# Kernel optimization log

Hardware: AMD Instinct MI355X
Metric: run time of the kernel (lower is better)

The kernel has to match this reference:

```python
import jax, jax.numpy as jnp
import numpy as np

N = 250000
E = 4000000
IN_F, HID, OUT = 18, 16, 1


def setup_inputs() -> dict:
    key = jax.random.key(0)
    ks = jax.random.split(key, 7)
    x = jax.random.normal(ks[0], (N, IN_F), dtype=jnp.float32)
    edge_index = jax.random.randint(ks[1], (2, E), 0, N, dtype=jnp.int64)
    # GCNConv params (PyG uses Glorot for weight, zeros for bias)
    W1 = jax.random.normal(ks[2], (IN_F, HID), dtype=jnp.float32) * (1.0 / np.sqrt(IN_F))
    b1 = jnp.zeros((HID,), dtype=jnp.float32)
    W2 = jax.random.normal(ks[3], (HID, OUT), dtype=jnp.float32) * (1.0 / np.sqrt(HID))
    b2 = jnp.zeros((OUT,), dtype=jnp.float32)
    return {"x": x, "edge_index": edge_index, "W1": W1, "b1": b1, "W2": W2, "b2": b2}


def _gcn_conv(x, W, b, src, dst, norm, n_nodes):
    # linear transform then degree-normalized scatter-add (PyG GCNConv)
    h = x @ W                                  # [N, F_out]
    msg = h[src] * norm[:, None]               # gather + per-edge scale
    out = jax.ops.segment_sum(msg, dst, num_segments=n_nodes)
    return out + b


def reference(x, edge_index, W1, b1, W2, b2):
    # add self-loops (GCNConv default add_self_loops=True)
    loops = jnp.arange(N, dtype=edge_index.dtype)
    src = jnp.concatenate([edge_index[0], loops])
    dst = jnp.concatenate([edge_index[1], loops])
    # symmetric normalization: deg computed at destination over self-looped graph
    deg = jax.ops.segment_sum(jnp.ones_like(dst, dtype=x.dtype), dst, num_segments=N)
    dis = jnp.where(deg > 0, jax.lax.rsqrt(deg), 0.0)
    norm = dis[src] * dis[dst]                 # [E+N]
    h = _gcn_conv(x, W1, b1, src, dst, norm, N)
    h = jax.nn.relu(h)
    # dropout is identity in eval mode (F.dropout(training=self.training))
    out = _gcn_conv(h, W2, b2, src, dst, norm, N)
    return out
```

## Files before the change

### kernel.cpp

```cpp
#include <hip/hip_runtime.h>
#include <hip/hip_fp16.h>


#define NB_BITS 8
#define BN (1 << NB_BITS)
#define NBINS 1024
#define BIN_TPB 512
#define BIN_CHUNK 8192
#define AGG_TPB 512
#define UF 8

__global__ void bhist_kernel(const int* __restrict__ dst, int* __restrict__ bcnt, int E) {
    __shared__ int cnt[NBINS];
    int t = threadIdx.x;
    for (int i = t; i < NBINS; i += BIN_TPB) cnt[i] = 0;
    __syncthreads();
    int base = blockIdx.x * BIN_CHUNK;
    int end = min(base + BIN_CHUNK, E);
#pragma unroll 4
    for (int e = base + t; e < end; e += BIN_TPB)
        atomicAdd(&cnt[dst[e] >> NB_BITS], 1);
    __syncthreads();
    for (int i = t; i < NBINS; i += BIN_TPB)
        if (cnt[i] > 0) atomicAdd(&bcnt[i], cnt[i]);
}

__global__ void bscan_kernel(const int* __restrict__ bcnt, int* __restrict__ bstart,
                             int* __restrict__ cursor) {
    __shared__ int s[NBINS];
    int t = threadIdx.x;
    int v = bcnt[t];
    s[t] = v;
    __syncthreads();
    for (int off = 1; off < NBINS; off <<= 1) {
        int add = (t >= off) ? s[t - off] : 0;
        __syncthreads();
        s[t] += add;
        __syncthreads();
    }
    int excl = s[t] - v;
    bstart[t] = excl;
    cursor[t] = excl;
    if (t == NBINS - 1) bstart[NBINS] = s[t];
}

__global__ void bplace_kernel(const int* __restrict__ src, const int* __restrict__ dst,
                              int* __restrict__ cursor, int* __restrict__ pairs, int E) {
    __shared__ int cnt[NBINS];
    int t = threadIdx.x;
    for (int i = t; i < NBINS; i += BIN_TPB) cnt[i] = 0;
    __syncthreads();
    int base = blockIdx.x * BIN_CHUNK;
    int end = min(base + BIN_CHUNK, E);
#pragma unroll 4
    for (int e = base + t; e < end; e += BIN_TPB)
        atomicAdd(&cnt[dst[e] >> NB_BITS], 1);
    __syncthreads();
    for (int i = t; i < NBINS; i += BIN_TPB) {
        int c = cnt[i];
        cnt[i] = (c > 0) ? atomicAdd(&cursor[i], c) : 0;
    }
    __syncthreads();
#pragma unroll 4
    for (int e = base + t; e < end; e += BIN_TPB) {
        int d = dst[e];
        int sv = src[e];
        int b = d >> NB_BITS;
        int p = atomicAdd(&cnt[b], 1);
        pairs[p] = (sv << NB_BITS) | (d & (BN - 1));
    }
}

__global__ void csr_kernel(const int* __restrict__ pairs, const int* __restrict__ bstart,
                           int* __restrict__ rowp, int* __restrict__ csr_src,
                           float* __restrict__ dis, int N) {
    __shared__ int cnt[BN];
    __shared__ int tmp[BN];
    int b = blockIdx.x, t = threadIdx.x;
    int s0 = bstart[b], s1 = bstart[b + 1];
    for (int i = t; i < BN; i += blockDim.x) cnt[i] = 0;
    __syncthreads();
#pragma unroll 4
    for (int e = s0 + t; e < s1; e += blockDim.x)
        atomicAdd(&cnt[pairs[e] & (BN - 1)], 1);
    __syncthreads();
    int v = (t < BN) ? cnt[t] : 0;
    if (t < BN) tmp[t] = v;
    __syncthreads();
    for (int off = 1; off < BN; off <<= 1) {
        int add = (t < BN && t >= off) ? tmp[t - off] : 0;
        __syncthreads();
        if (t < BN) tmp[t] += add;
        __syncthreads();
    }
    int nbase = b << NB_BITS;
    if (t < BN) {
        int start = s0 + tmp[t] - v;
        rowp[nbase + t] = start;
        int n = nbase + t;
        if (n < N) dis[n] = rsqrtf((float)v + 1.0f);
        cnt[t] = start;
    }
    if (t == 0) rowp[nbase + BN] = s1;
    __syncthreads();
#pragma unroll 4
    for (int e = s0 + t; e < s1; e += blockDim.x) {
        int pv = pairs[e];
        int pos = atomicAdd(&cnt[pv & (BN - 1)], 1);
        csr_src[pos] = pv >> NB_BITS;
    }
}

__global__ void h1_kernel(const float* __restrict__ x, const float* __restrict__ W1,
                          const float* __restrict__ dis, __half* __restrict__ hs1h, int N) {
    __shared__ float w[18 * 16];
    for (int i = threadIdx.x; i < 18 * 16; i += blockDim.x) w[i] = W1[i];
    __syncthreads();
    int n = blockIdx.x * blockDim.x + threadIdx.x;
    if (n >= N) return;
    const float2* x2 = (const float2*)(x + (size_t)n * 18);
    float xv[18];
#pragma unroll
    for (int k = 0; k < 9; k++) {
        float2 v = x2[k];
        xv[2 * k] = v.x;
        xv[2 * k + 1] = v.y;
    }
    float d = dis[n];
    float acc[16];
#pragma unroll
    for (int f = 0; f < 16; f++) acc[f] = 0.0f;
#pragma unroll
    for (int k = 0; k < 18; k++) {
        float xk = xv[k];
#pragma unroll
        for (int f = 0; f < 16; f++) acc[f] = fmaf(xk, w[k * 16 + f], acc[f]);
    }
    unsigned int u[8];
#pragma unroll
    for (int q = 0; q < 8; q++) {
        unsigned int lo = __half_as_ushort(__float2half_rn(acc[2 * q] * d));
        unsigned int hi = __half_as_ushort(__float2half_rn(acc[2 * q + 1] * d));
        u[q] = lo | (hi << 16);
    }
    uint4* outp = (uint4*)(hs1h + (size_t)n * 16);
    outp[0] = make_uint4(u[0], u[1], u[2], u[3]);
    outp[1] = make_uint4(u[4], u[5], u[6], u[7]);
}

__global__ void agg1_kernel(const int* __restrict__ csr_src, const int* __restrict__ rowp,
                            const __half* __restrict__ hs1h, const float* __restrict__ dis,
                            const float* __restrict__ b1, const float* __restrict__ W2,
                            float* __restrict__ hs2, int N) {
    int b = blockIdx.x, t = threadIdx.x;
    int f = t & 15;
    int g = t >> 4;
    float bbf = b1[f], wwf = W2[f];
    int nbase = b << NB_BITS;
    for (int nl = g; nl < BN; nl += AGG_TPB / 16) {
        int n = nbase + nl;
        if (n >= N) continue;
        int r0 = rowp[n], r1 = rowp[n + 1];
        float a = 0.f;
#pragma unroll 4
        for (int r = r0; r < r1; ++r) {
            int s = csr_src[r];
            a += __half2float(hs1h[(size_t)s * 16 + f]);
        }
        float d = dis[n];
        float self = __half2float(hs1h[(size_t)n * 16 + f]);
        float p = fmaxf(d * (a + self) + bbf, 0.f) * wwf;
        p += __shfl_xor(p, 1);
        p += __shfl_xor(p, 2);
        p += __shfl_xor(p, 4);
        p += __shfl_xor(p, 8);
        if (f == 0) hs2[n] = p * d;
    }
}

__global__ void agg2_kernel(const int* __restrict__ csr_src, const int* __restrict__ rowp,
                            const float* __restrict__ hs2, const float* __restrict__ dis,
                            const float* __restrict__ b2, float* __restrict__ out, int N) {
    int b = blockIdx.x, t = threadIdx.x;
    int l = t & 15;
    int g = t >> 4;
    int nbase = b << NB_BITS;
    float bb = b2[0];
    for (int nl = g; nl < BN; nl += AGG_TPB / 16) {
        int n = nbase + nl;
        if (n >= N) continue;
        int r0 = rowp[n], r1 = rowp[n + 1];
        float a = 0.f;
        for (int r = r0 + l; r < r1; r += 16) a += hs2[csr_src[r]];
        a += __shfl_xor(a, 1);
        a += __shfl_xor(a, 2);
        a += __shfl_xor(a, 4);
        a += __shfl_xor(a, 8);
        if (l == 0) out[n] = dis[n] * (a + hs2[n]) + bb;
    }
}

extern "C" void kernel_launch(void* const* d_in, const int* in_sizes, int n_in,
                              void* d_out, int out_size, void* d_ws, size_t ws_size,
                              hipStream_t stream) {
    const float* x = (const float*)d_in[0];
    const int* edge_index = (const int*)d_in[1];
    const float* W1 = (const float*)d_in[2];
    const float* b1 = (const float*)d_in[3];
    const float* W2 = (const float*)d_in[4];
    const float* b2 = (const float*)d_in[5];
    float* out = (float*)d_out;

    const int N = in_sizes[0] / 18;
    const int E = in_sizes[1] / 2;
    const int* src = edge_index;
    const int* dst = edge_index + E;
    const int NBUCKET = (N + BN - 1) / BN;

    int* ws = (int*)d_ws;
    int* pairs = ws;
    int* csr_src = pairs + (size_t)E;
    __half* hs1h = (__half*)(csr_src + (size_t)E);
    float* hs2 = (float*)((int*)(csr_src + (size_t)E) + 8 * (size_t)N);
    float* dis = hs2 + N;
    int* rowp = (int*)(dis + N);
    int* bstart = rowp + (size_t)NBUCKET * BN + 1;
    int* cursor = bstart + NBINS + 1;
    int* bcnt = cursor + NBINS;

    hipMemsetAsync(bcnt, 0, NBINS * sizeof(int), stream);

    int binBlocks = (E + BIN_CHUNK - 1) / BIN_CHUNK;
    int nBlocksN = (N + 255) / 256;

    bhist_kernel<<<binBlocks, BIN_TPB, 0, stream>>>(dst, bcnt, E);
    bscan_kernel<<<1, NBINS, 0, stream>>>(bcnt, bstart, cursor);
    bplace_kernel<<<binBlocks, BIN_TPB, 0, stream>>>(src, dst, cursor, pairs, E);
    csr_kernel<<<NBUCKET, 512, 0, stream>>>(pairs, bstart, rowp, csr_src, dis, N);
    h1_kernel<<<nBlocksN, 256, 0, stream>>>(x, W1, dis, hs1h, N);
    agg1_kernel<<<NBUCKET, AGG_TPB, 0, stream>>>(csr_src, rowp, hs1h, dis, b1, W2, hs2, N);
    agg2_kernel<<<NBUCKET, AGG_TPB, 0, stream>>>(csr_src, rowp, hs2, dis, b2, out, N);
}
```

Baseline: 276.8 us.

## Stage bucket placement in LDS and coarsen CSR buckets to 512 nodes

The binning pass now uses 512 coarse buckets of 512 nodes each, so each CSR block handles 512 nodes with one thread per node. In the placement kernel each block first sorts its chunk into LDS by bucket, using a local scan and per-bucket cursors. It then writes each bucket's entries as contiguous runs to global memory instead of scattering one word per edge. The aim is more coalesced writes and fewer global cursor atomics, at the cost of roughly 48KB of LDS per block (lower occupancy), an extra in-block scan, and more sync. The aggregation kernels keep 256-node blocks, which still works because rowp is indexed by node.

Result: faster. 254.1 us (-8.2%).

```diff
diff --git a/kernel.cpp b/kernel.cpp
--- a/kernel.cpp
+++ b/kernel.cpp
@@ -4,35 +4,35 @@
 
 #define NB_BITS 8
 #define BN (1 << NB_BITS)
-#define NBINS 1024
+#define SB_BITS 9
+#define SBN (1 << SB_BITS)
+#define NSB 512
 #define BIN_TPB 512
 #define BIN_CHUNK 8192
 #define AGG_TPB 512
-#define UF 8
 
 __global__ void bhist_kernel(const int* __restrict__ dst, int* __restrict__ bcnt, int E) {
-    __shared__ int cnt[NBINS];
+    __shared__ int cnt[NSB];
     int t = threadIdx.x;
-    for (int i = t; i < NBINS; i += BIN_TPB) cnt[i] = 0;
+    cnt[t] = 0;
     __syncthreads();
     int base = blockIdx.x * BIN_CHUNK;
     int end = min(base + BIN_CHUNK, E);
 #pragma unroll 4
     for (int e = base + t; e < end; e += BIN_TPB)
-        atomicAdd(&cnt[dst[e] >> NB_BITS], 1);
-    __syncthreads();
-    for (int i = t; i < NBINS; i += BIN_TPB)
-        if (cnt[i] > 0) atomicAdd(&bcnt[i], cnt[i]);
+        atomicAdd(&cnt[dst[e] >> SB_BITS], 1);
+    __syncthreads();
+    if (cnt[t] > 0) atomicAdd(&bcnt[t], cnt[t]);
 }
 
 __global__ void bscan_kernel(const int* __restrict__ bcnt, int* __restrict__ bstart,
                              int* __restrict__ cursor) {
-    __shared__ int s[NBINS];
+    __shared__ int s[NSB];
     int t = threadIdx.x;
     int v = bcnt[t];
     s[t] = v;
     __syncthreads();
-    for (int off = 1; off < NBINS; off <<= 1) {
+    for (int off = 1; off < NSB; off <<= 1) {
         int add = (t >= off) ? s[t - off] : 0;
         __syncthreads();
         s[t] += add;
@@ -41,73 +41,92 @@
     int excl = s[t] - v;
     bstart[t] = excl;
     cursor[t] = excl;
-    if (t == NBINS - 1) bstart[NBINS] = s[t];
+    if (t == NSB - 1) bstart[NSB] = s[t];
 }
 
 __global__ void bplace_kernel(const int* __restrict__ src, const int* __restrict__ dst,
                               int* __restrict__ cursor, int* __restrict__ pairs, int E) {
-    __shared__ int cnt[NBINS];
+    __shared__ int cnt[NSB];
+    __shared__ int lstart[NSB];
+    __shared__ int lcur[NSB];
+    __shared__ int gbase[NSB];
+    __shared__ int lbuf[BIN_CHUNK];
+    __shared__ unsigned short lbin[BIN_CHUNK];
     int t = threadIdx.x;
-    for (int i = t; i < NBINS; i += BIN_TPB) cnt[i] = 0;
-    __syncthreads();
     int base = blockIdx.x * BIN_CHUNK;
     int end = min(base + BIN_CHUNK, E);
+    cnt[t] = 0;
+    __syncthreads();
 #pragma unroll 4
     for (int e = base + t; e < end; e += BIN_TPB)
-        atomicAdd(&cnt[dst[e] >> NB_BITS], 1);
-    __syncthreads();
-    for (int i = t; i < NBINS; i += BIN_TPB) {
-        int c = cnt[i];
-        cnt[i] = (c > 0) ? atomicAdd(&cursor[i], c) : 0;
-    }
-    __syncthreads();
-#pragma unroll 4
+        atomicAdd(&cnt[dst[e] >> SB_BITS], 1);
+    __syncthreads();
+    int v = cnt[t];
+    lstart[t] = v;
+    __syncthreads();
+    for (int off = 1; off < NSB; off <<= 1) {
+        int add = (t >= off) ? lstart[t - off] : 0;
+        __syncthreads();
+        lstart[t] += add;
+        __syncthreads();
+    }
+    int excl = lstart[t] - v;
+    lstart[t] = excl;
+    lcur[t] = excl;
+    gbase[t] = (v > 0) ? atomicAdd(&cursor[t], v) : 0;
+    __syncthreads();
+#pragma unroll 2
     for (int e = base + t; e < end; e += BIN_TPB) {
-        int d = dst[e];
-        int sv = src[e];
-        int b = d >> NB_BITS;
-        int p = atomicAdd(&cnt[b], 1);
-        pairs[p] = (sv << NB_BITS) | (d & (BN - 1));
+        int d = dst[e], s = src[e];
+        int b = d >> SB_BITS;
+        int pos = atomicAdd(&lcur[b], 1);
+        lbuf[pos] = (s << SB_BITS) | (d & (SBN - 1));
+        lbin[pos] = (unsigned short)b;
+    }
+    __syncthreads();
+    int n = end - base;
+#pragma unroll 4
+    for (int i = t; i < n; i += BIN_TPB) {
+        int b = lbin[i];
+        pairs[gbase[b] + (i - lstart[b])] = lbuf[i];
     }
 }
 
 __global__ void csr_kernel(const int* __restrict__ pairs, const int* __restrict__ bstart,
                            int* __restrict__ rowp, int* __restrict__ csr_src,
                            float* __restrict__ dis, int N) {
-    __shared__ int cnt[BN];
-    __shared__ int tmp[BN];
+    __shared__ int cnt[SBN];
+    __shared__ int tmp[SBN];
     int b = blockIdx.x, t = threadIdx.x;
     int s0 = bstart[b], s1 = bstart[b + 1];
-    for (int i = t; i < BN; i += blockDim.x) cnt[i] = 0;
-    __syncthreads();
-#pragma unroll 4
-    for (int e = s0 + t; e < s1; e += blockDim.x)
-        atomicAdd(&cnt[pairs[e] & (BN - 1)], 1);
-    __syncthreads();
-    int v = (t < BN) ? cnt[t] : 0;
-    if (t < BN) tmp[t] = v;
-    __syncthreads();
-    for (int off = 1; off < BN; off <<= 1) {
-        int add = (t < BN && t >= off) ? tmp[t - off] : 0;
-        __syncthreads();
-        if (t < BN) tmp[t] += add;
-        __syncthreads();
-    }
-    int nbase = b << NB_BITS;
-    if (t < BN) {
-        int start = s0 + tmp[t] - v;
-        rowp[nbase + t] = start;
-        int n = nbase + t;
-        if (n < N) dis[n] = rsqrtf((float)v + 1.0f);
-        cnt[t] = start;
-    }
-    if (t == 0) rowp[nbase + BN] = s1;
-    __syncthreads();
-#pragma unroll 4
-    for (int e = s0 + t; e < s1; e += blockDim.x) {
+    cnt[t] = 0;
+    __syncthreads();
+#pragma unroll 4
+    for (int e = s0 + t; e < s1; e += SBN)
+        atomicAdd(&cnt[pairs[e] & (SBN - 1)], 1);
+    __syncthreads();
+    int v = cnt[t];
+    tmp[t] = v;
+    __syncthreads();
+    for (int off = 1; off < SBN; off <<= 1) {
+        int add = (t >= off) ? tmp[t - off] : 0;
+        __syncthreads();
+        tmp[t] += add;
+        __syncthreads();
+    }
+    int nbase = b << SB_BITS;
+    int start = s0 + tmp[t] - v;
+    rowp[nbase + t] = start;
+    int n = nbase + t;
+    if (n < N) dis[n] = rsqrtf((float)v + 1.0f);
+    cnt[t] = start;
+    if (t == 0) rowp[nbase + SBN] = s1;
+    __syncthreads();
+#pragma unroll 4
+    for (int e = s0 + t; e < s1; e += SBN) {
         int pv = pairs[e];
-        int pos = atomicAdd(&cnt[pv & (BN - 1)], 1);
-        csr_src[pos] = pv >> NB_BITS;
+        int pos = atomicAdd(&cnt[pv & (SBN - 1)], 1);
+        csr_src[pos] = pv >> SB_BITS;
     }
 }
 
@@ -215,7 +234,8 @@
     const int E = in_sizes[1] / 2;
     const int* src = edge_index;
     const int* dst = edge_index + E;
-    const int NBUCKET = (N + BN - 1) / BN;
+    const int NABUCKET = (N + BN - 1) / BN;
+    const int NSBUCKET = (N + SBN - 1) / SBN;
 
     int* ws = (int*)d_ws;
     int* pairs = ws;
@@ -224,20 +244,20 @@
     float* hs2 = (float*)((int*)(csr_src + (size_t)E) + 8 * (size_t)N);
     float* dis = hs2 + N;
     int* rowp = (int*)(dis + N);
-    int* bstart = rowp + (size_t)NBUCKET * BN + 1;
-    int* cursor = bstart + NBINS + 1;
-    int* bcnt = cursor + NBINS;
-
-    hipMemsetAsync(bcnt, 0, NBINS * sizeof(int), stream);
+    int* bstart = rowp + (size_t)NSBUCKET * SBN + 1;
+    int* cursor = bstart + NSB + 1;
+    int* bcnt = cursor + NSB;
+
+    hipMemsetAsync(bcnt, 0, NSB * sizeof(int), stream);
 
     int binBlocks = (E + BIN_CHUNK - 1) / BIN_CHUNK;
     int nBlocksN = (N + 255) / 256;
 
     bhist_kernel<<<binBlocks, BIN_TPB, 0, stream>>>(dst, bcnt, E);
-    bscan_kernel<<<1, NBINS, 0, stream>>>(bcnt, bstart, cursor);
+    bscan_kernel<<<1, NSB, 0, stream>>>(bcnt, bstart, cursor);
     bplace_kernel<<<binBlocks, BIN_TPB, 0, stream>>>(src, dst, cursor, pairs, E);
-    csr_kernel<<<NBUCKET, 512, 0, stream>>>(pairs, bstart, rowp, csr_src, dis, N);
+    csr_kernel<<<NSBUCKET, SBN, 0, stream>>>(pairs, bstart, rowp, csr_src, dis, N);
     h1_kernel<<<nBlocksN, 256, 0, stream>>>(x, W1, dis, hs1h, N);
-    agg1_kernel<<<NBUCKET, AGG_TPB, 0, stream>>>(csr_src, rowp, hs1h, dis, b1, W2, hs2, N);
-    agg2_kernel<<<NBUCKET, AGG_TPB, 0, stream>>>(csr_src, rowp, hs2, dis, b2, out, N);
-}
+    agg1_kernel<<<NABUCKET, AGG_TPB, 0, stream>>>(csr_src, rowp, hs1h, dis, b1, W2, hs2, N);
+    agg2_kernel<<<NABUCKET, AGG_TPB, 0, stream>>>(csr_src, rowp, hs2, dis, b2, out, N);
+}
```
